# Performance work log

Hardware: AMD Instinct MI355X
Metric: run time of the kernel (lower is better)

## Reference

```python
import jax, jax.numpy as jnp
import numpy as np
from jax import lax

PS = 16            # patch_size
QT = 0.7           # quality_threshold
SAP = 0.8          # strong_aug_prob
PDP = 0.1          # patch_drop_prob


def setup_inputs() -> dict:
    key = jax.random.key(0)
    ks = jax.random.split(key, 10)
    B, C, H, W = 32, 1, 1024, 1024
    pH, pW = H // PS, W // PS
    img = jax.random.uniform(ks[0], (B, C, H, W), jnp.float32)
    noise = jax.random.normal(ks[1], (B, C, H, W), jnp.float32)
    r_strong = jax.random.uniform(ks[2], (pH, pW), jnp.float32)
    r_drop = jax.random.uniform(ks[3], (pH, pW), jnp.float32)
    r_else = jax.random.uniform(ks[4], (pH, pW), jnp.float32)
    bright_f = jax.random.uniform(ks[5], (pH, pW), jnp.float32, minval=0.7, maxval=1.3)
    contrast_f = jax.random.uniform(ks[6], (pH, pW), jnp.float32, minval=0.7, maxval=1.3)
    slight_f = jax.random.uniform(ks[7], (pH, pW), jnp.float32, minval=0.9, maxval=1.1)
    aug_choice = jax.random.randint(ks[8], (pH, pW), 0, 4, jnp.int32)
    slight_choice = jax.random.randint(ks[9], (pH, pW), 0, 2, jnp.int32)
    return dict(img=img, noise=noise, r_strong=r_strong, r_drop=r_drop,
                r_else=r_else, bright_f=bright_f, contrast_f=contrast_f,
                slight_f=slight_f, aug_choice=aug_choice, slight_choice=slight_choice)


def _forward(img, noise, r_strong, r_drop, r_else, bright_f, contrast_f,
             slight_f, aug_choice, slight_choice):
    B, C, H, W = img.shape
    pH, pW = H // PS, W // PS
    # (B, C, pH, pW, PS, PS) patch view
    p6 = img.reshape(B, C, pH, PS, pW, PS).transpose(0, 1, 2, 4, 3, 5)
    flat = p6.reshape(B, C, pH, pW, PS * PS)
    mean_i = flat.mean(-1)
    var = flat.var(-1, ddof=1)          # torch .var/.std are unbiased
    std = jnp.sqrt(var)
    intensity_q = 1.0 - 2.0 * jnp.abs(mean_i - 0.5)
    quality = (std + intensity_q + var) / 3.0   # (B, C, pH, pW)
    q = quality.squeeze(1).mean(0)               # batch-mean quality per patch (pH, pW)

    low = q < QT
    strong = low & (r_strong < SAP)
    drop = low & (q < 0.3) & (r_drop < PDP)
    els = (~low) & (r_else < 0.3)

    # per-patch action code: 0=identity, 1=noise, 2=blur, 3=brightness,
    # 4=contrast, 5=slight_noise, 6=slight_brightness, 7=drop
    code = jnp.where(strong, aug_choice + 1, 0)
    code = jnp.where(els, slight_choice + 5, code)
    code = jnp.where(drop, 7, code)

    up = lambda m: jnp.repeat(jnp.repeat(m, PS, axis=0), PS, axis=1)  # (pH,pW)->(H,W)
    cu = up(code)[None, None]

    # candidate augmented images (patches are disjoint, so compute globally + mask)
    noise_img = jnp.clip(img + noise * 0.1, 0.0, 1.0)
    # per-patch 3x3 avg pool with zero padding confined to each patch
    blur6 = lax.reduce_window(p6, 0.0, lax.add,
                              (1, 1, 1, 1, 3, 3), (1, 1, 1, 1, 1, 1),
                              [(0, 0)] * 4 + [(1, 1), (1, 1)]) / 9.0
    blur_img = blur6.transpose(0, 1, 2, 4, 3, 5).reshape(B, C, H, W)
    bright_img = jnp.clip(img * up(bright_f)[None, None], 0.0, 1.0)
    m_pp = up(p6.mean(axis=(0, 1, 4, 5)))[None, None]   # patch.mean() over B,C,PS,PS
    cf = up(contrast_f)[None, None]
    contrast_img = jnp.clip((img - m_pp) * cf + m_pp, 0.0, 1.0)
    snoise_img = jnp.clip(img + noise * 0.05, 0.0, 1.0)
    sbright_img = jnp.clip(img * up(slight_f)[None, None], 0.0, 1.0)

    out = jnp.where(cu == 1, noise_img, img)
    out = jnp.where(cu == 2, blur_img, out)
    out = jnp.where(cu == 3, bright_img, out)
    out = jnp.where(cu == 4, contrast_img, out)
    out = jnp.where(cu == 5, snoise_img, out)
    out = jnp.where(cu == 6, sbright_img, out)
    out = jnp.where(cu == 7, 0.0, out)
    return out


def reference(img, noise, r_strong, r_drop, r_else, bright_f, contrast_f,
              slight_f, aug_choice, slight_choice):
    return _forward(img, noise, r_strong, r_drop, r_else, bright_f,
                    contrast_f, slight_f, aug_choice, slight_choice)
```

## Files before the change

### kernel.cpp

```cpp
#include <hip/hip_runtime.h>
#include <math.h>

#define PS 16
#define PH 64
#define PWD 64
#define NB 32
#define IW 1024
#define IH 1024
#define NPATCH (PH*PWD)

__device__ __forceinline__ float clamp01(float v) {
    return fminf(fmaxf(v, 0.0f), 1.0f);
}

__global__ __launch_bounds__(256) void stats_kernel(const float* __restrict__ img,
                                                    float* __restrict__ ws_mean,
                                                    float* __restrict__ ws_qual) {
    const int blk = blockIdx.x;
    const int b  = blk >> 6;
    const int ph = blk & 63;
    const int t  = threadIdx.x;

    size_t base = ((size_t)b * IH + (size_t)ph * PS) * IW + (size_t)t * 4;
    float s = 0.0f, ss = 0.0f;
#pragma unroll
    for (int i = 0; i < PS; ++i) {
        float4 v = *(const float4*)(img + base + (size_t)i * IW);
        s  += v.x + v.y + v.z + v.w;
        ss += v.x * v.x + v.y * v.y + v.z * v.z + v.w * v.w;
    }
    s  += __shfl_xor(s, 1);  ss += __shfl_xor(ss, 1);
    s  += __shfl_xor(s, 2);  ss += __shfl_xor(ss, 2);

    if ((t & 3) == 0) {
        float mean = s * (1.0f / 256.0f);
        float var  = (ss - s * s * (1.0f / 256.0f)) * (1.0f / 255.0f);
        var = fmaxf(var, 0.0f);
        float sd   = sqrtf(var);
        float iq   = 1.0f - 2.0f * fabsf(mean - 0.5f);
        float qual = (sd + iq + var) * (1.0f / 3.0f);
        int p = ph * PWD + (t >> 2);
        ws_mean[b * NPATCH + p] = mean;
        ws_qual[b * NPATCH + p] = qual;
    }
}

__global__ __launch_bounds__(256) void decide_kernel(const float* __restrict__ ws_mean,
                                                     const float* __restrict__ ws_qual,
                                                     const float* __restrict__ r_strong,
                                                     const float* __restrict__ r_drop,
                                                     const float* __restrict__ r_else,
                                                     const float* __restrict__ bright_f,
                                                     const float* __restrict__ contrast_f,
                                                     const float* __restrict__ slight_f,
                                                     const int* __restrict__ aug_choice,
                                                     const int* __restrict__ slight_choice,
                                                     int* __restrict__ ws_op,
                                                     float* __restrict__ ws_a,
                                                     float* __restrict__ ws_b) {
    int p = blockIdx.x * 256 + threadIdx.x;
    if (p >= NPATCH) return;
    float qs = 0.0f, ms = 0.0f;
    for (int b = 0; b < NB; ++b) {
        qs += ws_qual[b * NPATCH + p];
        ms += ws_mean[b * NPATCH + p];
    }
    float q   = qs * (1.0f / (float)NB);
    float mpp = ms * (1.0f / (float)NB);

    bool low    = q < 0.7f;
    bool strong = low && (r_strong[p] < 0.8f);
    bool drop   = low && (q < 0.3f) && (r_drop[p] < 0.1f);
    bool els    = (!low) && (r_else[p] < 0.3f);

    int code = strong ? (aug_choice[p] + 1) : 0;
    if (els)  code = slight_choice[p] + 5;
    if (drop) code = 7;

    int op = 0; float a = 0.0f, bb = 0.0f;
    switch (code) {
        case 1: op = 1; a = 0.1f;  break;
        case 5: op = 1; a = 0.05f; break;
        case 2: op = 2; break;
        case 3: op = 3; a = bright_f[p]; bb = 0.0f; break;
        case 6: op = 3; a = slight_f[p]; bb = 0.0f; break;
        case 4: { op = 3; float cf = contrast_f[p];
                  a = cf; bb = mpp - mpp * cf; break; }
        case 7: op = 4; break;
        default: break;
    }
    ws_op[p] = op; ws_a[p] = a; ws_b[p] = bb;
}

__global__ __launch_bounds__(256) void apply_kernel(const float* __restrict__ img,
                                                    const float* __restrict__ noise,
                                                    const int* __restrict__ ws_op,
                                                    const float* __restrict__ ws_a,
                                                    const float* __restrict__ ws_b,
                                                    float* __restrict__ out) {
    __shared__ float strip[PS][IW];
    const int blk = blockIdx.x;
    const int b  = blk >> 6;
    const int ph = blk & 63;
    const int t  = threadIdx.x;

    size_t base = ((size_t)b * IH + (size_t)ph * PS) * IW + (size_t)t * 4;
    float4* sv = (float4*)&strip[0][0];
#pragma unroll
    for (int i = 0; i < PS; ++i) {
        sv[i * 256 + t] = *(const float4*)(img + base + (size_t)i * IW);
    }
    __syncthreads();

    const int pp = ph * PWD + (t >> 2);
    const int op = ws_op[pp];
    const float a  = ws_a[pp];
    const float bb = ws_b[pp];
    const int w0 = t * 4;

    for (int i = 0; i < PS; ++i) {
        float4 x = sv[i * 256 + t];
        float4 y;
        if (op == 0) {
            y = x;
        } else if (op == 3) {
            y.x = clamp01(fmaf(x.x, a, bb));
            y.y = clamp01(fmaf(x.y, a, bb));
            y.z = clamp01(fmaf(x.z, a, bb));
            y.w = clamp01(fmaf(x.w, a, bb));
        } else if (op == 1) {
            float4 n = *(const float4*)(noise + base + (size_t)i * IW);
            y.x = clamp01(fmaf(n.x, a, x.x));
            y.y = clamp01(fmaf(n.y, a, x.y));
            y.z = clamp01(fmaf(n.z, a, x.z));
            y.w = clamp01(fmaf(n.w, a, x.w));
        } else if (op == 4) {
            y.x = y.y = y.z = y.w = 0.0f;
        } else {
            float vs[6];
#pragma unroll
            for (int c = 0; c < 6; ++c) {
                int col = w0 - 1 + c;
                bool valid = true;
                if (c == 0) valid = (t & 3) != 0;
                if (c == 5) valid = (t & 3) != 3;
                float sc = 0.0f;
                if (valid) {
                    if (i > 0)      sc += strip[i - 1][col];
                    sc += strip[i][col];
                    if (i < PS - 1) sc += strip[i + 1][col];
                }
                vs[c] = sc;
            }
            y.x = (vs[0] + vs[1] + vs[2]) / 9.0f;
            y.y = (vs[1] + vs[2] + vs[3]) / 9.0f;
            y.z = (vs[2] + vs[3] + vs[4]) / 9.0f;
            y.w = (vs[3] + vs[4] + vs[5]) / 9.0f;
        }
        *(float4*)(out + base + (size_t)i * IW) = y;
    }
}

extern "C" void kernel_launch(void* const* d_in, const int* in_sizes, int n_in,
                              void* d_out, int out_size, void* d_ws, size_t ws_size,
                              hipStream_t stream) {
    const float* img        = (const float*)d_in[0];
    const float* noise      = (const float*)d_in[1];
    const float* r_strong   = (const float*)d_in[2];
    const float* r_drop     = (const float*)d_in[3];
    const float* r_else     = (const float*)d_in[4];
    const float* bright_f   = (const float*)d_in[5];
    const float* contrast_f = (const float*)d_in[6];
    const float* slight_f   = (const float*)d_in[7];
    const int*   aug_choice    = (const int*)d_in[8];
    const int*   slight_choice = (const int*)d_in[9];
    float* out = (float*)d_out;

    float* ws      = (float*)d_ws;
    float* ws_mean = ws;
    float* ws_qual = ws + NB * NPATCH;
    int*   ws_op   = (int*)(ws + 2 * NB * NPATCH);
    float* ws_a    = ws + 2 * NB * NPATCH + NPATCH;
    float* ws_b    = ws + 2 * NB * NPATCH + 2 * NPATCH;

    stats_kernel<<<NB * PH, 256, 0, stream>>>(img, ws_mean, ws_qual);
    decide_kernel<<<NPATCH / 256, 256, 0, stream>>>(ws_mean, ws_qual,
        r_strong, r_drop, r_else, bright_f, contrast_f, slight_f,
        aug_choice, slight_choice, ws_op, ws_a, ws_b);
    apply_kernel<<<NB * PH, 256, 0, stream>>>(img, noise, ws_op, ws_a, ws_b, out);
}
```

Baseline: 384.2 us.

## Drop shared-memory strip staging in apply kernel, use register rolling blur

The apply kernel no longer stages a 64KB strip of 16 rows into LDS for every block. Non-blur patches now stream rows straight from global memory. Blur patches keep a rolling three-row window in registers and get the horizontal neighbours from adjacent lanes with shuffles. This removes the large LDS allocation, which limited occupancy, and the block-wide barrier, at the cost of per-lane branching inside a wave. The 3x3 blur is still computed exactly, with zero padding at patch edges.

New measurement: 375.4 us. 2.3% less time.

```diff
diff --git a/kernel.cpp b/kernel.cpp
--- a/kernel.cpp
+++ b/kernel.cpp
@@ -98,66 +98,68 @@
                                                     const float* __restrict__ ws_a,
                                                     const float* __restrict__ ws_b,
                                                     float* __restrict__ out) {
-    __shared__ float strip[PS][IW];
     const int blk = blockIdx.x;
     const int b  = blk >> 6;
     const int ph = blk & 63;
     const int t  = threadIdx.x;
 
-    size_t base = ((size_t)b * IH + (size_t)ph * PS) * IW + (size_t)t * 4;
-    float4* sv = (float4*)&strip[0][0];
-#pragma unroll
-    for (int i = 0; i < PS; ++i) {
-        sv[i * 256 + t] = *(const float4*)(img + base + (size_t)i * IW);
-    }
-    __syncthreads();
+    const size_t base = ((size_t)b * IH + (size_t)ph * PS) * IW + (size_t)t * 4;
 
     const int pp = ph * PWD + (t >> 2);
     const int op = ws_op[pp];
     const float a  = ws_a[pp];
     const float bb = ws_b[pp];
-    const int w0 = t * 4;
 
-    for (int i = 0; i < PS; ++i) {
-        float4 x = sv[i * 256 + t];
-        float4 y;
-        if (op == 0) {
-            y = x;
-        } else if (op == 3) {
-            y.x = clamp01(fmaf(x.x, a, bb));
-            y.y = clamp01(fmaf(x.y, a, bb));
-            y.z = clamp01(fmaf(x.z, a, bb));
-            y.w = clamp01(fmaf(x.w, a, bb));
-        } else if (op == 1) {
-            float4 n = *(const float4*)(noise + base + (size_t)i * IW);
-            y.x = clamp01(fmaf(n.x, a, x.x));
-            y.y = clamp01(fmaf(n.y, a, x.y));
-            y.z = clamp01(fmaf(n.z, a, x.z));
-            y.w = clamp01(fmaf(n.w, a, x.w));
-        } else if (op == 4) {
-            y.x = y.y = y.z = y.w = 0.0f;
-        } else {
-            float vs[6];
-#pragma unroll
-            for (int c = 0; c < 6; ++c) {
-                int col = w0 - 1 + c;
-                bool valid = true;
-                if (c == 0) valid = (t & 3) != 0;
-                if (c == 5) valid = (t & 3) != 3;
-                float sc = 0.0f;
-                if (valid) {
-                    if (i > 0)      sc += strip[i - 1][col];
-                    sc += strip[i][col];
-                    if (i < PS - 1) sc += strip[i + 1][col];
-                }
-                vs[c] = sc;
+    if (op != 2) {
+#pragma unroll 4
+        for (int i = 0; i < PS; ++i) {
+            float4 x = *(const float4*)(img + base + (size_t)i * IW);
+            float4 y;
+            if (op == 1) {
+                float4 n = *(const float4*)(noise + base + (size_t)i * IW);
+                y.x = clamp01(fmaf(n.x, a, x.x));
+                y.y = clamp01(fmaf(n.y, a, x.y));
+                y.z = clamp01(fmaf(n.z, a, x.z));
+                y.w = clamp01(fmaf(n.w, a, x.w));
+            } else if (op == 3) {
+                y.x = clamp01(fmaf(x.x, a, bb));
+                y.y = clamp01(fmaf(x.y, a, bb));
+                y.z = clamp01(fmaf(x.z, a, bb));
+                y.w = clamp01(fmaf(x.w, a, bb));
+            } else if (op == 4) {
+                y.x = y.y = y.z = y.w = 0.0f;
+            } else {
+                y = x;
             }
-            y.x = (vs[0] + vs[1] + vs[2]) / 9.0f;
-            y.y = (vs[1] + vs[2] + vs[3]) / 9.0f;
-            y.z = (vs[2] + vs[3] + vs[4]) / 9.0f;
-            y.w = (vs[3] + vs[4] + vs[5]) / 9.0f;
+            *(float4*)(out + base + (size_t)i * IW) = y;
         }
-        *(float4*)(out + base + (size_t)i * IW) = y;
+    }
+    if (op == 2) {
+        const bool left_edge  = (t & 3) == 0;
+        const bool right_edge = (t & 3) == 3;
+        float4 prev = make_float4(0.f, 0.f, 0.f, 0.f);
+        float4 cur  = *(const float4*)(img + base);
+        float4 next;
+        for (int i = 0; i < PS; ++i) {
+            if (i < PS - 1) next = *(const float4*)(img + base + (size_t)(i + 1) * IW);
+            else            next = make_float4(0.f, 0.f, 0.f, 0.f);
+            float4 v;
+            v.x = prev.x + cur.x + next.x;
+            v.y = prev.y + cur.y + next.y;
+            v.z = prev.z + cur.z + next.z;
+            v.w = prev.w + cur.w + next.w;
+            float left  = __shfl_up(v.w, 1);
+            float right = __shfl_down(v.x, 1);
+            if (left_edge)  left  = 0.0f;
+            if (right_edge) right = 0.0f;
+            float4 y;
+            y.x = (left + v.x + v.y) * (1.0f / 9.0f);
+            y.y = (v.x + v.y + v.z) * (1.0f / 9.0f);
+            y.z = (v.y + v.z + v.w) * (1.0f / 9.0f);
+            y.w = (v.z + v.w + right) * (1.0f / 9.0f);
+            *(float4*)(out + base + (size_t)i * IW) = y;
+            prev = cur; cur = next;
+        }
     }
 }
 
```
